# Kernel tuning notes

Hardware: AMD Instinct MI355X
Metric: run time of the kernel (lower is better)

The kernel has to match this reference:

```python
import jax, jax.numpy as jnp
import numpy as np

N_NODES = 50000
E_EDGES = 1600000
D = 256


def setup_inputs() -> dict:
    key = jax.random.key(0)
    ks = jax.random.split(key, 10)
    inp = {
        "x": jax.random.normal(ks[0], (N_NODES, D), dtype=jnp.float32),
        "W0": jax.random.normal(ks[1], (D, D), dtype=jnp.float32) * (1.0 / np.sqrt(D)),
        "W1": jax.random.normal(ks[2], (D, D), dtype=jnp.float32) * (1.0 / np.sqrt(D)),
        "b": jnp.zeros((D,), dtype=jnp.float32),
        "src0": jax.random.randint(ks[3], (E_EDGES,), 0, N_NODES, dtype=jnp.int32),
        "dst0": jax.random.randint(ks[4], (E_EDGES,), 0, N_NODES, dtype=jnp.int32),
        "val0": jax.random.uniform(ks[5], (E_EDGES,), dtype=jnp.float32),
        "src1": jax.random.randint(ks[6], (E_EDGES,), 0, N_NODES, dtype=jnp.int32),
        "dst1": jax.random.randint(ks[7], (E_EDGES,), 0, N_NODES, dtype=jnp.int32),
        "val1": jax.random.uniform(ks[8], (E_EDGES,), dtype=jnp.float32),
    }
    return inp


def _spmm(src, dst, val, dense, num_segments):
    # sparse [N,N] (COO: A[dst, src] = val) @ dense [N,D] -> [N,D]
    # gather rows of dense at src, scale by edge value, scatter-add to dst
    return jax.ops.segment_sum(val[:, None] * dense[src], dst, num_segments=num_segments)


def reference(x, W0, W1, b, src0, dst0, val0, src1, dst1, val1):
    n = x.shape[0]
    # per-support dense GEMM then SpMM, summed over supports (2 supports)
    out = _spmm(src0, dst0, val0, x @ W0, n)
    out = out + _spmm(src1, dst1, val1, x @ W1, n)
    out = out + b  # bias
    return jax.nn.relu(out)  # act = F.relu
```

## Files before the change

### kernel.cpp

```cpp
#include <hip/hip_runtime.h>

#define D 256
#define K2 512
#define CAP 64
#define CAP_S 60
#define OVFCAP 16384
#define BCAP 10240
#define CHUNK 8192

typedef __attribute__((ext_vector_type(8))) short short8;
typedef __attribute__((ext_vector_type(4))) float f32x4;

__device__ inline ushort f2bf(float f) {
  unsigned u = __float_as_uint(f);
  unsigned r = (u + 0x7FFF + ((u >> 16) & 1)) >> 16;
  return (ushort)r;
}
__device__ inline float bf_lo(unsigned u) { return __uint_as_float(u << 16); }
__device__ inline float bf_hi(unsigned u) { return __uint_as_float(u & 0xFFFF0000u); }

__global__ __launch_bounds__(256) void prep_kernel(const float* __restrict__ W0,
                                                   const float* __restrict__ W1,
                                                   ushort* __restrict__ Wt,
                                                   int* __restrict__ gz, int ngz) {
  if (blockIdx.x < 128) {
    const int blk = blockIdx.x;
    const float* W = (blk >> 6) ? W1 : W0;
    const int koff = (blk >> 6) ? 256 : 0;
    __shared__ float t[32][33];
    int tx = threadIdx.x & 31, ty = threadIdx.x >> 5;
    int b = blk & 63;
    int k0 = (b & 7) * 32, n0 = (b >> 3) * 32;
    for (int r = ty; r < 32; r += 8)
      t[r][tx] = W[(size_t)(k0 + r) * D + n0 + tx];
    __syncthreads();
    for (int r = ty; r < 32; r += 8)
      Wt[(size_t)(n0 + r) * K2 + koff + k0 + tx] = f2bf(t[tx][r]);
  } else {
    int nb = gridDim.x - 128;
    for (int i = (blockIdx.x - 128) * 256 + threadIdx.x; i < ngz; i += nb * 256)
      gz[i] = 0;
  }
}

__device__ __forceinline__ void binA_body(const int* __restrict__ src,
                                          const int* __restrict__ dst,
                                          const float* __restrict__ val, int E,
                                          int* __restrict__ gcur,
                                          int2* __restrict__ binned,
                                          int* __restrict__ ovfc, int4* __restrict__ ovf,
                                          int nbkt, int blk) {
  __shared__ int hist[200];
  __shared__ int base[200];
  const int tid = threadIdx.x;
  for (int i = tid; i < nbkt; i += 256) hist[i] = 0;
  __syncthreads();
  const int e0 = blk * CHUNK;
  const int e1 = min(E, e0 + CHUNK);
  for (int e = e0 + tid; e < e1; e += 256)
    atomicAdd(&hist[dst[e] >> 8], 1);
  __syncthreads();
  for (int i = tid; i < nbkt; i += 256) {
    int h = hist[i];
    base[i] = h ? atomicAdd(&gcur[i], h) : 0;
    hist[i] = 0;
  }
  __syncthreads();
  for (int e = e0 + tid; e < e1; e += 256) {
    int d = dst[e];
    int s = src[e];
    int vb = __float_as_int(val[e]);
    int k = d >> 8;
    int pos = base[k] + atomicAdd(&hist[k], 1);
    if (pos < BCAP) {
      binned[(size_t)k * BCAP + pos] = make_int2(((d & 255) << 16) | s, vb);
    } else {
      int o = atomicAdd(ovfc, 1);
      if (o < OVFCAP) ovf[o] = make_int4(d, s, vb, 0);
    }
  }
}

__global__ __launch_bounds__(256) void fat_kernel(
    const float* __restrict__ x, ushort* __restrict__ Xb, int nq,
    const int* __restrict__ src0, const int* __restrict__ dst0, const float* __restrict__ val0,
    int E0, int* __restrict__ gcur0, int2* __restrict__ binned0, int* __restrict__ ovfc0,
    int4* __restrict__ ovf0,
    const int* __restrict__ src1, const int* __restrict__ dst1, const float* __restrict__ val1,
    int E1, int* __restrict__ gcur1, int2* __restrict__ binned1, int* __restrict__ ovfc1,
    int4* __restrict__ ovf1,
    int nbkt, int nbA0, int nbA1) {
  const int bid = blockIdx.x;
  if (bid < nbA0) {
    binA_body(src0, dst0, val0, E0, gcur0, binned0, ovfc0, ovf0, nbkt, bid);
  } else if (bid < nbA0 + nbA1) {
    binA_body(src1, dst1, val1, E1, gcur1, binned1, ovfc1, ovf1, nbkt, bid - nbA0);
  } else {
    const int nxb = gridDim.x - nbA0 - nbA1;
    for (int i = (bid - nbA0 - nbA1) * 256 + threadIdx.x; i < nq; i += nxb * 256) {
      float4 v = ((const float4*)x)[i];
      ushort4 o;
      o.x = f2bf(v.x); o.y = f2bf(v.y); o.z = f2bf(v.z); o.w = f2bf(v.w);
      ((ushort4*)Xb)[i] = o;
    }
  }
}

__device__ __forceinline__ void passB_body(const int2* __restrict__ binned,
                                           const int* __restrict__ gcur,
                                           uint* __restrict__ padded,
                                           int* __restrict__ cnt,
                                           int* __restrict__ ovfc, int4* __restrict__ ovf,
                                           int b) {
  __shared__ int lcnt[256];
  __shared__ uint stage[256 * CAP_S];
  const int tid = threadIdx.x;
  lcnt[tid] = 0;
  __syncthreads();
  const int n = min(gcur[b], BCAP);
  const int2* bp = binned + (size_t)b * BCAP;
  for (int i = tid; i < n; i += 256) {
    int2 e = bp[i];
    int dlow = (e.x >> 16) & 255;
    int s = atomicAdd(&lcnt[dlow], 1);
    if (s < CAP_S) {
      float v = __int_as_float(e.y);
      stage[dlow * CAP_S + s] = (uint)(e.x & 0xFFFF) | ((uint)f2bf(v) << 16);
    } else {
      int o = atomicAdd(ovfc, 1);
      if (o < OVFCAP) ovf[o] = make_int4((b << 8) + dlow, e.x & 0xFFFF, e.y, 0);
    }
  }
  __syncthreads();
  const int row = (b << 8) + tid;
  const int written = min(lcnt[tid], CAP_S);
  cnt[row] = written;
  const int nq = (written + 3) >> 2;
  for (int s = written; s < (nq << 2); ++s) stage[tid * CAP_S + s] = 0;
  uint4* dp = (uint4*)(padded + ((size_t)row << 6));
  const uint4* sp = (const uint4*)&stage[tid * CAP_S];
  for (int q = 0; q < nq; ++q) dp[q] = sp[q];
}

__global__ __launch_bounds__(256) void passBoth(
    const int2* __restrict__ binned0, const int* __restrict__ gcur0, uint* __restrict__ padded0,
    int* __restrict__ cnt0, int* __restrict__ ovfc0, int4* __restrict__ ovf0,
    const int2* __restrict__ binned1, const int* __restrict__ gcur1, uint* __restrict__ padded1,
    int* __restrict__ cnt1, int* __restrict__ ovfc1, int4* __restrict__ ovf1, int nbkt) {
  if (blockIdx.x < nbkt)
    passB_body(binned0, gcur0, padded0, cnt0, ovfc0, ovf0, blockIdx.x);
  else
    passB_body(binned1, gcur1, padded1, cnt1, ovfc1, ovf1, blockIdx.x - nbkt);
}

__device__ __forceinline__ void gather_acc(const ushort* __restrict__ H,
                                           const uint* __restrict__ padded,
                                           int row, int c, int lane, float4& acc) {
  const int nc = (c + 3) >> 2;
  if (nc <= 0) return;
  const uint4* ep4 = (const uint4*)(padded + ((size_t)row << 6));
  const uint2* Hl = (const uint2*)H + lane;

  uint2 h0[4], h1[4];
  float v0[4], v1[4];

#define GA_ISSUE(S, J)                                                  \
  do {                                                                  \
    uint4 m = ep4[(J)];                                                 \
    uint ee[4] = {m.x, m.y, m.z, m.w};                                  \
    _Pragma("unroll") for (int k = 0; k < 4; ++k) {                     \
      v##S[k] = __uint_as_float(ee[k] & 0xFFFF0000u);                   \
      h##S[k] = Hl[(size_t)(ee[k] & 0xFFFFu) << 6];                     \
    }                                                                   \
  } while (0)

#define GA_COMP(S)                                                      \
  do {                                                                  \
    _Pragma("unroll") for (int k = 0; k < 4; ++k) {                     \
      acc.x += v##S[k] * bf_lo(h##S[k].x);                              \
      acc.y += v##S[k] * bf_hi(h##S[k].x);                              \
      acc.z += v##S[k] * bf_lo(h##S[k].y);                              \
      acc.w += v##S[k] * bf_hi(h##S[k].y);                              \
    }                                                                   \
  } while (0)

  GA_ISSUE(0, 0);
  if (nc > 1) GA_ISSUE(1, 1);
  int j = 0;
  for (; j + 1 < nc; j += 2) {
    GA_COMP(0);
    if (j + 2 < nc) GA_ISSUE(0, j + 2);
    GA_COMP(1);
    if (j + 3 < nc) GA_ISSUE(1, j + 3);
  }
  if (j < nc) GA_COMP(0);
#undef GA_ISSUE
#undef GA_COMP
}

__global__ __launch_bounds__(256) void spmmY(const ushort* __restrict__ Xb,
                                             const uint* __restrict__ padded0,
                                             const int* __restrict__ cnt0,
                                             const uint* __restrict__ padded1,
                                             const int* __restrict__ cnt1,
                                             ushort* __restrict__ Y, int N) {
  const int row = blockIdx.x * 4 + (threadIdx.x >> 6);
  if (row >= N) return;
  const int lane = threadIdx.x & 63;
  float4 a0 = make_float4(0.f, 0.f, 0.f, 0.f);
  float4 a1 = make_float4(0.f, 0.f, 0.f, 0.f);
  gather_acc(Xb, padded0, row, min(cnt0[row], CAP), lane, a0);
  gather_acc(Xb, padded1, row, min(cnt1[row], CAP), lane, a1);
  ushort4 o0, o1;
  o0.x = f2bf(a0.x); o0.y = f2bf(a0.y); o0.z = f2bf(a0.z); o0.w = f2bf(a0.w);
  o1.x = f2bf(a1.x); o1.y = f2bf(a1.y); o1.z = f2bf(a1.z); o1.w = f2bf(a1.w);
  *(ushort4*)(Y + (size_t)row * K2 + 4 * lane) = o0;
  *(ushort4*)(Y + (size_t)row * K2 + 256 + 4 * lane) = o1;
}

__global__ void ovf_serial(const int* __restrict__ ovfc0, const int4* __restrict__ ovf0,
                           const int* __restrict__ ovfc1, const int4* __restrict__ ovf1,
                           const ushort* __restrict__ Xb, ushort* __restrict__ Y) {
  int n0 = min(*ovfc0, OVFCAP);
  int n1 = min(*ovfc1, OVFCAP);
  const int tid = threadIdx.x;
  for (int i = 0; i < n0 + n1; ++i) {
    int4 r = (i < n0) ? ovf0[i] : ovf1[i - n0];
    int koff = (i < n0) ? 0 : 256;
    float v = __int_as_float(r.z);
    size_t yo = (size_t)r.x * K2 + koff + tid;
    float y = __uint_as_float((uint)Y[yo] << 16);
    float xv = __uint_as_float((uint)Xb[(size_t)r.y * D + tid] << 16);
    Y[yo] = f2bf(y + v * xv);
    __syncthreads();
  }
}

__global__ __launch_bounds__(256) void gemm_out(const ushort* __restrict__ Y,
                                                const ushort* __restrict__ Wt,
                                                float* __restrict__ out,
                                                const float* __restrict__ bias,
                                                int M, int mtiles) {
  __shared__ ushort As[128 * 40];
  __shared__ ushort Bs[128 * 40];
  const int tid = threadIdx.x;
  const int blk = blockIdx.x;
  const int bm = (blk % mtiles) * 128;
  const int bn = (blk / mtiles) * 128;
  const int wave = tid >> 6, lane = tid & 63;
  const int wm = wave & 1, wn = wave >> 1;
  const int lr = lane & 15;
  const int kg = lane >> 4;
  f32x4 acc[4][4];
#pragma unroll
  for (int m = 0; m < 4; ++m)
#pragma unroll
    for (int n = 0; n < 4; ++n) acc[m][n] = (f32x4){0.f, 0.f, 0.f, 0.f};

  for (int k0 = 0; k0 < K2; k0 += 32) {
    __syncthreads();
#pragma unroll
    for (int c = 0; c < 2; ++c) {
      int linear = c * 256 + tid;
      int row = linear >> 2;
      int part = linear & 3;
      int gr = bm + row;
      uint4 a4 = make_uint4(0u, 0u, 0u, 0u);
      if (gr < M) a4 = *(const uint4*)(Y + (size_t)gr * K2 + k0 + part * 8);
      *(uint4*)&As[row * 40 + part * 8] = a4;
    }
#pragma unroll
    for (int c = 0; c < 2; ++c) {
      int linear = c * 256 + tid;
      int row = linear >> 2;
      int part = linear & 3;
      uint4 w4 = *(const uint4*)(Wt + (size_t)(bn + row) * K2 + k0 + part * 8);
      *(uint4*)&Bs[row * 40 + part * 8] = w4;
    }
    __syncthreads();
    short8 af[4], bfr[4];
#pragma unroll
    for (int m = 0; m < 4; ++m)
      af[m] = *(const short8*)&As[(wm * 64 + m * 16 + lr) * 40 + kg * 8];
#pragma unroll
    for (int n = 0; n < 4; ++n)
      bfr[n] = *(const short8*)&Bs[(wn * 64 + n * 16 + lr) * 40 + kg * 8];
#pragma unroll
    for (int m = 0; m < 4; ++m)
#pragma unroll
      for (int n = 0; n < 4; ++n)
        acc[m][n] = __builtin_amdgcn_mfma_f32_16x16x32_bf16(af[m], bfr[n], acc[m][n], 0, 0, 0);
  }

#pragma unroll
  for (int m = 0; m < 4; ++m)
#pragma unroll
    for (int j = 0; j < 4; ++j) {
      int gr = bm + wm * 64 + m * 16 + kg * 4 + j;
      if (gr < M) {
#pragma unroll
        for (int n = 0; n < 4; ++n) {
          int gc = bn + wn * 64 + n * 16 + lr;
          out[(size_t)gr * D + gc] = fmaxf(acc[m][n][j] + bias[gc], 0.f);
        }
      }
    }
}

extern "C" void kernel_launch(void* const* d_in, const int* in_sizes, int n_in,
                              void* d_out, int out_size, void* d_ws, size_t ws_size,
                              hipStream_t stream) {
  const float* x    = (const float*)d_in[0];
  const float* W0   = (const float*)d_in[1];
  const float* W1   = (const float*)d_in[2];
  const float* b    = (const float*)d_in[3];
  const int*   src0 = (const int*)d_in[4];
  const int*   dst0 = (const int*)d_in[5];
  const float* val0 = (const float*)d_in[6];
  const int*   src1 = (const int*)d_in[7];
  const int*   dst1 = (const int*)d_in[8];
  const float* val1 = (const float*)d_in[9];
  float* out = (float*)d_out;

  const int N  = in_sizes[0] / D;
  const int E0 = in_sizes[4];
  const int E1 = in_sizes[7];
  const int nbkt = (N + 255) >> 8;
  const int nrows = nbkt << 8;

  const int mtiles = (N + 127) / 128;
  const int NGB = mtiles * 2;
  const int nbA0 = (E0 + CHUNK - 1) / CHUNK;
  const int nbA1 = (E1 + CHUNK - 1) / CHUNK;
  const int NXB = 224;
  const int NPB = (N + 3) / 4;

  size_t off = 0;
  auto alloc = [&](size_t bytes) -> void* {
    void* p = (char*)d_ws + off;
    off = (off + bytes + 255) & ~(size_t)255;
    return p;
  };
  ushort* Xb      = (ushort*)alloc((size_t)N * D * 2);
  ushort* Wt      = (ushort*)alloc((size_t)D * K2 * 2);
  uint*   padded0 = (uint*)alloc((size_t)nrows * CAP * 4);
  uint*   padded1 = (uint*)alloc((size_t)nrows * CAP * 4);
  int*    cnt0    = (int*)alloc((size_t)nrows * 4);
  int*    cnt1    = (int*)alloc((size_t)nrows * 4);
  int*    gzall   = (int*)alloc((size_t)(2 * nbkt + 2) * 4);
  int4*   ovf0    = (int4*)alloc((size_t)OVFCAP * 16);
  int4*   ovf1    = (int4*)alloc((size_t)OVFCAP * 16);
  int2*   binned0 = (int2*)alloc((size_t)nbkt * BCAP * 8);
  int2*   binned1 = (int2*)alloc((size_t)nbkt * BCAP * 8);
  ushort* Y       = (ushort*)binned0;

  int* gcur0 = gzall;
  int* gcur1 = gzall + nbkt;
  int* ovfc0 = gzall + 2 * nbkt;
  int* ovfc1 = gzall + 2 * nbkt + 1;

  prep_kernel<<<130, 256, 0, stream>>>(W0, W1, Wt, gzall, 2 * nbkt + 2);
  fat_kernel<<<nbA0 + nbA1 + NXB, 256, 0, stream>>>(
      x, Xb, N * D / 4,
      src0, dst0, val0, E0, gcur0, binned0, ovfc0, ovf0,
      src1, dst1, val1, E1, gcur1, binned1, ovfc1, ovf1,
      nbkt, nbA0, nbA1);
  passBoth<<<2 * nbkt, 256, 0, stream>>>(binned0, gcur0, padded0, cnt0, ovfc0, ovf0,
                                         binned1, gcur1, padded1, cnt1, ovfc1, ovf1, nbkt);
  spmmY<<<NPB, 256, 0, stream>>>(Xb, padded0, cnt0, padded1, cnt1, Y, N);
  ovf_serial<<<1, 256, 0, stream>>>(ovfc0, ovf0, ovfc1, ovf1, Xb, Y);
  gemm_out<<<NGB, 256, 0, stream>>>(Y, Wt, out, b, N, mtiles);
}
```

Before: 322.1 us.

## Fuse SpMM gather with output GEMM and move overflow edges into pre-pass

The gathered bf16 aggregate Y is no longer written to global memory. Each block gathers 16 rows into swizzled shared memory and immediately multiplies them by the concatenated weights with MFMA, then applies bias and ReLU. Overflow edges are now handled by a single-block pre-kernel that computes their partial output contributions and flags the affected rows, so the fused kernel can add those partials. This removes the Y round trip and one launch, but each block rereads the full weight matrix from global or L2 memory with only 16 rows of reuse, and the overflow path is a serial scalar dot product.

```diff
diff --git a/kernel.cpp b/kernel.cpp
--- a/kernel.cpp
+++ b/kernel.cpp
@@ -198,113 +198,102 @@
 #undef GA_COMP
 }
 
-__global__ __launch_bounds__(256) void spmmY(const ushort* __restrict__ Xb,
-                                             const uint* __restrict__ padded0,
-                                             const int* __restrict__ cnt0,
-                                             const uint* __restrict__ padded1,
-                                             const int* __restrict__ cnt1,
-                                             ushort* __restrict__ Y, int N) {
-  const int row = blockIdx.x * 4 + (threadIdx.x >> 6);
-  if (row >= N) return;
-  const int lane = threadIdx.x & 63;
-  float4 a0 = make_float4(0.f, 0.f, 0.f, 0.f);
-  float4 a1 = make_float4(0.f, 0.f, 0.f, 0.f);
-  gather_acc(Xb, padded0, row, min(cnt0[row], CAP), lane, a0);
-  gather_acc(Xb, padded1, row, min(cnt1[row], CAP), lane, a1);
-  ushort4 o0, o1;
-  o0.x = f2bf(a0.x); o0.y = f2bf(a0.y); o0.z = f2bf(a0.z); o0.w = f2bf(a0.w);
-  o1.x = f2bf(a1.x); o1.y = f2bf(a1.y); o1.z = f2bf(a1.z); o1.w = f2bf(a1.w);
-  *(ushort4*)(Y + (size_t)row * K2 + 4 * lane) = o0;
-  *(ushort4*)(Y + (size_t)row * K2 + 256 + 4 * lane) = o1;
-}
-
-__global__ void ovf_serial(const int* __restrict__ ovfc0, const int4* __restrict__ ovf0,
-                           const int* __restrict__ ovfc1, const int4* __restrict__ ovf1,
-                           const ushort* __restrict__ Xb, ushort* __restrict__ Y) {
+__global__ __launch_bounds__(256) void spmm_fused(
+    const ushort* __restrict__ Xb,
+    const uint* __restrict__ padded0, const int* __restrict__ cnt0,
+    const uint* __restrict__ padded1, const int* __restrict__ cnt1,
+    const ushort* __restrict__ Wt, float* __restrict__ out,
+    const float* __restrict__ bias, const int* __restrict__ rowflag, int N) {
+  __shared__ ushort As[16 * 512];
+  const int tid = threadIdx.x;
+  const int wave = tid >> 6, lane = tid & 63;
+  const int brow = blockIdx.x * 16;
+
+  for (int rr = 0; rr < 4; ++rr) {
+    const int r = wave * 4 + rr;
+    const int row = brow + r;
+    float4 a0 = make_float4(0.f, 0.f, 0.f, 0.f);
+    float4 a1 = make_float4(0.f, 0.f, 0.f, 0.f);
+    if (row < N) {
+      gather_acc(Xb, padded0, row, min(cnt0[row], CAP), lane, a0);
+      gather_acc(Xb, padded1, row, min(cnt1[row], CAP), lane, a1);
+    }
+    ushort4 o0, o1;
+    o0.x = f2bf(a0.x); o0.y = f2bf(a0.y); o0.z = f2bf(a0.z); o0.w = f2bf(a0.w);
+    o1.x = f2bf(a1.x); o1.y = f2bf(a1.y); o1.z = f2bf(a1.z); o1.w = f2bf(a1.w);
+    const int sw = r & 7;
+    {
+      int c0 = 4 * lane;
+      int cb = (c0 >> 3) ^ sw;
+      *(ushort4*)&As[r * 512 + (cb << 3) + (c0 & 7)] = o0;
+    }
+    {
+      int c0 = 256 + 4 * lane;
+      int cb = (c0 >> 3) ^ sw;
+      *(ushort4*)&As[r * 512 + (cb << 3) + (c0 & 7)] = o1;
+    }
+  }
+  __syncthreads();
+
+  const int lr = lane & 15;
+  const int kg = lane >> 4;
+  f32x4 acc[4];
+#pragma unroll
+  for (int n = 0; n < 4; ++n) acc[n] = (f32x4){0.f, 0.f, 0.f, 0.f};
+  const ushort* Wn = Wt + (size_t)(wave * 64) * K2;
+  const int asw = lr & 7;
+#pragma unroll 4
+  for (int ks = 0; ks < 16; ++ks) {
+    const int cb = (4 * ks + kg) ^ asw;
+    short8 af = *(const short8*)&As[lr * 512 + (cb << 3)];
+#pragma unroll
+    for (int n = 0; n < 4; ++n) {
+      short8 bfr = *(const short8*)(Wn + (size_t)(n * 16 + lr) * K2 + ks * 32 + kg * 8);
+      acc[n] = __builtin_amdgcn_mfma_f32_16x16x32_bf16(af, bfr, acc[n], 0, 0, 0);
+    }
+  }
+
+#pragma unroll
+  for (int j = 0; j < 4; ++j) {
+    const int gr = brow + kg * 4 + j;
+    if (gr < N) {
+      const bool flagged = rowflag[gr] != 0;
+#pragma unroll
+      for (int n = 0; n < 4; ++n) {
+        const int gc = wave * 64 + n * 16 + lr;
+        float base = 0.f;
+        if (flagged) base = out[(size_t)gr * D + gc];
+        out[(size_t)gr * D + gc] = fmaxf(acc[n][j] + bias[gc] + base, 0.f);
+      }
+    }
+  }
+}
+
+__global__ void ovf_fix(const int* __restrict__ ovfc0, const int4* __restrict__ ovf0,
+                        const int* __restrict__ ovfc1, const int4* __restrict__ ovf1,
+                        const ushort* __restrict__ Xb, const ushort* __restrict__ Wt,
+                        float* __restrict__ out, int* __restrict__ rowflag) {
   int n0 = min(*ovfc0, OVFCAP);
   int n1 = min(*ovfc1, OVFCAP);
-  const int tid = threadIdx.x;
-  for (int i = 0; i < n0 + n1; ++i) {
+  int nt = n0 + n1;
+  if (nt == 0) return;
+  const int t = threadIdx.x;
+  for (int i = 0; i < nt; ++i) {
+    int4 r = (i < n0) ? ovf0[i] : ovf1[i - n0];
+    if (t == 0) rowflag[r.x] = 1;
+    out[(size_t)r.x * D + t] = 0.f;
+  }
+  __syncthreads();
+  for (int i = 0; i < nt; ++i) {
     int4 r = (i < n0) ? ovf0[i] : ovf1[i - n0];
     int koff = (i < n0) ? 0 : 256;
     float v = __int_as_float(r.z);
-    size_t yo = (size_t)r.x * K2 + koff + tid;
-    float y = __uint_as_float((uint)Y[yo] << 16);
-    float xv = __uint_as_float((uint)Xb[(size_t)r.y * D + tid] << 16);
-    Y[yo] = f2bf(y + v * xv);
-    __syncthreads();
-  }
-}
-
-__global__ __launch_bounds__(256) void gemm_out(const ushort* __restrict__ Y,
-                                                const ushort* __restrict__ Wt,
-                                                float* __restrict__ out,
-                                                const float* __restrict__ bias,
-                                                int M, int mtiles) {
-  __shared__ ushort As[128 * 40];
-  __shared__ ushort Bs[128 * 40];
-  const int tid = threadIdx.x;
-  const int blk = blockIdx.x;
-  const int bm = (blk % mtiles) * 128;
-  const int bn = (blk / mtiles) * 128;
-  const int wave = tid >> 6, lane = tid & 63;
-  const int wm = wave & 1, wn = wave >> 1;
-  const int lr = lane & 15;
-  const int kg = lane >> 4;
-  f32x4 acc[4][4];
-#pragma unroll
-  for (int m = 0; m < 4; ++m)
-#pragma unroll
-    for (int n = 0; n < 4; ++n) acc[m][n] = (f32x4){0.f, 0.f, 0.f, 0.f};
-
-  for (int k0 = 0; k0 < K2; k0 += 32) {
-    __syncthreads();
-#pragma unroll
-    for (int c = 0; c < 2; ++c) {
-      int linear = c * 256 + tid;
-      int row = linear >> 2;
-      int part = linear & 3;
-      int gr = bm + row;
-      uint4 a4 = make_uint4(0u, 0u, 0u, 0u);
-      if (gr < M) a4 = *(const uint4*)(Y + (size_t)gr * K2 + k0 + part * 8);
-      *(uint4*)&As[row * 40 + part * 8] = a4;
-    }
-#pragma unroll
-    for (int c = 0; c < 2; ++c) {
-      int linear = c * 256 + tid;
-      int row = linear >> 2;
-      int part = linear & 3;
-      uint4 w4 = *(const uint4*)(Wt + (size_t)(bn + row) * K2 + k0 + part * 8);
-      *(uint4*)&Bs[row * 40 + part * 8] = w4;
-    }
-    __syncthreads();
-    short8 af[4], bfr[4];
-#pragma unroll
-    for (int m = 0; m < 4; ++m)
-      af[m] = *(const short8*)&As[(wm * 64 + m * 16 + lr) * 40 + kg * 8];
-#pragma unroll
-    for (int n = 0; n < 4; ++n)
-      bfr[n] = *(const short8*)&Bs[(wn * 64 + n * 16 + lr) * 40 + kg * 8];
-#pragma unroll
-    for (int m = 0; m < 4; ++m)
-#pragma unroll
-      for (int n = 0; n < 4; ++n)
-        acc[m][n] = __builtin_amdgcn_mfma_f32_16x16x32_bf16(af[m], bfr[n], acc[m][n], 0, 0, 0);
-  }
-
-#pragma unroll
-  for (int m = 0; m < 4; ++m)
-#pragma unroll
-    for (int j = 0; j < 4; ++j) {
-      int gr = bm + wm * 64 + m * 16 + kg * 4 + j;
-      if (gr < M) {
-#pragma unroll
-        for (int n = 0; n < 4; ++n) {
-          int gc = bn + wn * 64 + n * 16 + lr;
-          out[(size_t)gr * D + gc] = fmaxf(acc[m][n][j] + bias[gc], 0.f);
-        }
-      }
-    }
+    float s = 0.f;
+    for (int k = 0; k < 256; ++k)
+      s += __uint_as_float((uint)Xb[(size_t)r.y * D + k] << 16) *
+           __uint_as_float((uint)Wt[(size_t)t * K2 + koff + k] << 16);
+    out[(size_t)r.x * D + t] += v * s;
+  }
 }
 
 extern "C" void kernel_launch(void* const* d_in, const int* in_sizes, int n_in,
@@ -328,12 +317,10 @@
   const int nbkt = (N + 255) >> 8;
   const int nrows = nbkt << 8;
 
-  const int mtiles = (N + 127) / 128;
-  const int NGB = mtiles * 2;
   const int nbA0 = (E0 + CHUNK - 1) / CHUNK;
   const int nbA1 = (E1 + CHUNK - 1) / CHUNK;
   const int NXB = 224;
-  const int NPB = (N + 3) / 4;
+  const int NFB = (N + 15) / 16;
 
   size_t off = 0;
   auto alloc = [&](size_t bytes) -> void* {
@@ -347,19 +334,20 @@
   uint*   padded1 = (uint*)alloc((size_t)nrows * CAP * 4);
   int*    cnt0    = (int*)alloc((size_t)nrows * 4);
   int*    cnt1    = (int*)alloc((size_t)nrows * 4);
-  int*    gzall   = (int*)alloc((size_t)(2 * nbkt + 2) * 4);
+  int*    gzall   = (int*)alloc((size_t)(2 * nbkt + 2 + nrows) * 4);
   int4*   ovf0    = (int4*)alloc((size_t)OVFCAP * 16);
   int4*   ovf1    = (int4*)alloc((size_t)OVFCAP * 16);
   int2*   binned0 = (int2*)alloc((size_t)nbkt * BCAP * 8);
   int2*   binned1 = (int2*)alloc((size_t)nbkt * BCAP * 8);
-  ushort* Y       = (ushort*)binned0;
-
-  int* gcur0 = gzall;
-  int* gcur1 = gzall + nbkt;
-  int* ovfc0 = gzall + 2 * nbkt;
-  int* ovfc1 = gzall + 2 * nbkt + 1;
-
-  prep_kernel<<<130, 256, 0, stream>>>(W0, W1, Wt, gzall, 2 * nbkt + 2);
+
+  int* gcur0   = gzall;
+  int* gcur1   = gzall + nbkt;
+  int* ovfc0   = gzall + 2 * nbkt;
+  int* ovfc1   = gzall + 2 * nbkt + 1;
+  int* rowflag = gzall + 2 * nbkt + 2;
+  const int ngz = 2 * nbkt + 2 + nrows;
+
+  prep_kernel<<<192, 256, 0, stream>>>(W0, W1, Wt, gzall, ngz);
   fat_kernel<<<nbA0 + nbA1 + NXB, 256, 0, stream>>>(
       x, Xb, N * D / 4,
       src0, dst0, val0, E0, gcur0, binned0, ovfc0, ovf0,
@@ -367,7 +355,7 @@
       nbkt, nbA0, nbA1);
   passBoth<<<2 * nbkt, 256, 0, stream>>>(binned0, gcur0, padded0, cnt0, ovfc0, ovf0,
                                          binned1, gcur1, padded1, cnt1, ovfc1, ovf1, nbkt);
-  spmmY<<<NPB, 256, 0, stream>>>(Xb, padded0, cnt0, padded1, cnt1, Y, N);
-  ovf_serial<<<1, 256, 0, stream>>>(ovfc0, ovf0, ovfc1, ovf1, Xb, Y);
-  gemm_out<<<NGB, 256, 0, stream>>>(Y, Wt, out, b, N, mtiles);
-}
+  ovf_fix<<<1, 256, 0, stream>>>(ovfc0, ovf0, ovfc1, ovf1, Xb, Wt, out, rowflag);
+  spmm_fused<<<NFB, 256, 0, stream>>>(Xb, padded0, cnt0, padded1, cnt1,
+                                      Wt, out, b, rowflag, N);
+}
```

Result: slower. 399.6 us (+24.1%).
